# Kernel tuning notes

Hardware: AMD Instinct MI355X
Metric: run time of the kernel (lower is better)

The kernel has to match this reference:

```python
import jax, jax.numpy as jnp
import numpy as np

B, T, S = 32, 64, 64
V, E, H, Hs = 32000, 512, 512, 512
D2 = 2 * Hs  # src feature dim


def setup_inputs() -> dict:
    key = jax.random.key(0)
    ks = jax.random.split(key, 26)
    n = lambda k, shape, s=0.05: (jax.random.normal(k, shape, jnp.float32) * s)
    inp = {
        'src': jax.random.normal(ks[0], (B, S, D2), jnp.float32),
        'trg': jax.random.randint(ks[1], (B, T), 0, V),
        'mask': jnp.ones((B, T), jnp.float32),
        'emb': n(ks[2], (V, E)),
        # PyTorch LSTMCell params: weight_ih [4H, E+H], weight_hh [4H, H]
        'f_Wih': n(ks[3], (4 * H, E + H)), 'f_Whh': n(ks[4], (4 * H, H)),
        'f_bih': n(ks[5], (4 * H,)), 'f_bhh': n(ks[6], (4 * H,)),
        'b_Wih': n(ks[7], (4 * H, E + H)), 'b_Whh': n(ks[8], (4 * H, H)),
        'b_bih': n(ks[9], (4 * H,)), 'b_bhh': n(ks[10], (4 * H,)),
        # attention projections: hidden -> 2*src_hidden
        'fatt_W': n(ks[11], (D2, H)), 'fatt_b': n(ks[12], (D2,)),
        'batt_W': n(ks[13], (D2, H)), 'batt_b': n(ks[14], (D2,)),
        # att_hidden linears: (H + 2*Hs) -> H
        'fah_W': n(ks[15], (H, H + D2)), 'fah_b': n(ks[16], (H,)),
        'bah_W': n(ks[17], (H, H + D2)), 'bah_b': n(ks[18], (H,)),
        # output projection 2H -> V
        'fc_W': n(ks[19], (V, 2 * H)), 'fc_b': n(ks[20], (V,)),
        'feed_init': n(ks[21], (2 * H,), 1.0),
        'hid_init': n(ks[22], (4 * H,), 1.0),
    }
    return inp


def reference(src, trg, mask, emb, f_Wih, f_Whh, f_bih, f_bhh,
              b_Wih, b_Whh, b_bih, b_bhh, fatt_W, fatt_b, batt_W, batt_b,
              fah_W, fah_b, bah_W, bah_b, fc_W, fc_b, feed_init, hid_init):
    Bn = src.shape[0]
    Hn = feed_init.shape[0] // 2
    scale = 1.0 / np.sqrt(Hn)  # key.size(-1) == trg hidden before projection

    x = emb[trg]  # [B, T, E]  (dropout p=0 -> identity)

    hhat0 = jnp.broadcast_to(feed_init, (Bn, 2 * Hn))
    f_hhat0, b_hhat0 = jnp.split(hhat0, 2, axis=1)
    hid0 = jnp.broadcast_to(hid_init, (Bn, 4 * Hn))
    f_hid, b_hid = jnp.split(hid0, 2, axis=-1)
    f_h0, f_c0 = jnp.split(f_hid, 2, axis=-1)
    b_h0, b_c0 = jnp.split(b_hid, 2, axis=-1)

    def lstm(xin, h, c, Wih, Whh, bih, bhh):
        g = xin @ Wih.T + bih + h @ Whh.T + bhh
        i, f, gg, o = jnp.split(g, 4, axis=-1)
        c = jax.nn.sigmoid(f) * c + jax.nn.sigmoid(i) * jnp.tanh(gg)
        h = jax.nn.sigmoid(o) * jnp.tanh(c)
        return h, c

    def att(h, W, b):
        k = h @ W.T + b                              # [B, 2Hs]
        w = jnp.einsum('bd,bsd->bs', k, src) * scale  # [B, S]
        p = jax.nn.softmax(w, axis=-1)
        return jnp.einsum('bs,bsd->bd', p, src)       # [B, 2Hs]

    xs = jnp.swapaxes(x, 0, 1)      # [T, B, E]
    ms = jnp.swapaxes(mask, 0, 1)   # [T, B]

    def f_step(carry, x_t):
        h, c, hhat = carry
        h, c = lstm(jnp.concatenate([x_t, hhat], -1), h, c, f_Wih, f_Whh, f_bih, f_bhh)
        ct = att(h, fatt_W, fatt_b)
        # NOTE: original uses b_att_hidden in the forward loop (faithful)
        hhat = jnp.tanh(jnp.concatenate([h, ct], -1) @ bah_W.T + bah_b)
        return (h, c, hhat), hhat

    _, f_out = jax.lax.scan(f_step, (f_h0, f_c0, f_hhat0), xs)  # [T, B, H]

    def b_step(carry, inp):
        x_t, m_t = inp
        h, c, hhat = carry
        hn, cn = lstm(jnp.concatenate([x_t, hhat], -1), h, c, b_Wih, b_Whh, b_bih, b_bhh)
        h = m_t[:, None] * hn
        c = m_t[:, None] * cn
        ct = att(h, batt_W, batt_b)
        # NOTE: original uses f_att_hidden in the backward loop (faithful)
        hhat = jnp.tanh(jnp.concatenate([h, ct], -1) @ fah_W.T + fah_b)
        return (h, c, hhat), hhat

    _, b_out = jax.lax.scan(b_step, (b_h0, b_c0, b_hhat0), (xs[::-1], ms[::-1]))

    f_out = jnp.swapaxes(f_out, 0, 1)        # [B, T, H]
    b_cheat = jnp.swapaxes(b_out, 0, 1)      # reversed-time order, as stacked in torch
    # b_outputs[:, :-2] = b_outputs_cheat[:, 2:]; last two steps zero (faithful)
    b_shift = jnp.concatenate([b_cheat[:, 2:], jnp.zeros_like(b_cheat[:, :2])], axis=1)

    logits = jnp.concatenate([f_out, b_shift], -1) @ fc_W.T + fc_b  # [B, T, V]
    return logits
```

## Files before the change

kernel.cpp:

```cpp
#include <hip/hip_runtime.h>
#include <hip/hip_bf16.h>
#include <math.h>

typedef __hip_bfloat16 bf16;
typedef __attribute__((ext_vector_type(8))) short short8b;
typedef __attribute__((ext_vector_type(8))) __bf16 bf16x8;
typedef __attribute__((ext_vector_type(4))) float f32x4;
typedef __attribute__((ext_vector_type(2))) unsigned u32x2;

#define SCALE_F 0.04419417382415922f

template <typename V>
static __device__ inline auto mfma_try(V a, V b, f32x4 c, int)
    -> decltype(__builtin_amdgcn_mfma_f32_16x16x32_bf16(a, b, c, 0, 0, 0)) {
  return __builtin_amdgcn_mfma_f32_16x16x32_bf16(a, b, c, 0, 0, 0);
}
template <typename V>
static __device__ inline auto mfma_try(V a, V b, f32x4 c, long)
    -> decltype(__builtin_amdgcn_mfma_f32_16x16x32_bf16(
        __builtin_bit_cast(bf16x8, a), __builtin_bit_cast(bf16x8, b), c, 0, 0, 0)) {
  return __builtin_amdgcn_mfma_f32_16x16x32_bf16(
      __builtin_bit_cast(bf16x8, a), __builtin_bit_cast(bf16x8, b), c, 0, 0, 0);
}
static __device__ inline f32x4 MFMA(short8b a, short8b b, f32x4 c) {
  return mfma_try(a, b, c, 0);
}

static __device__ inline short8b ldb8(const bf16* p) {
  return *reinterpret_cast<const short8b*>(p);
}
static __device__ inline float b2f(bf16 v) { return __bfloat162float(v); }
static __device__ inline bf16 f2b(float v) { return __float2bfloat16(v); }
static __device__ inline float s2f(short s) {
  unsigned u = ((unsigned)(unsigned short)s) << 16;
  return __builtin_bit_cast(float, u);
}
static __device__ inline unsigned pack2(float lo, float hi) {
  const unsigned a = (unsigned)__builtin_bit_cast(unsigned short, f2b(lo));
  const unsigned b = (unsigned)__builtin_bit_cast(unsigned short, f2b(hi));
  return a | (b << 16);
}
static __device__ inline float sigm(float x) { return 1.f / (1.f + expf(-x)); }

static __device__ inline void st4_wt(bf16* p, float lo, float hi) {
  unsigned ud = pack2(lo, hi);
  asm volatile("global_store_dword %0, %1, off sc0 sc1" ::"v"(p), "v"(ud)
               : "memory");
}
static __device__ inline void st8_wt(bf16* p, f32x4 v) {
  u32x2 ud;
  ud[0] = pack2(v[0], v[1]);
  ud[1] = pack2(v[2], v[3]);
  asm volatile("global_store_dwordx2 %0, %1, off sc0 sc1" ::"v"(p), "v"(ud)
               : "memory");
}

static __device__ inline void st_flag(unsigned* p, unsigned v) {
  asm volatile("global_store_dword %0, %1, off sc0 sc1" ::"v"(p), "v"(v)
               : "memory");
}
static __device__ inline unsigned ld_flag(const unsigned* p) {
  unsigned v;
  asm volatile("global_load_dword %0, %1, off sc0 sc1\n\ts_waitcnt vmcnt(0)"
               : "=v"(v)
               : "v"(p)
               : "memory");
  return v;
}

static __device__ inline void ld8_dw(
    const unsigned* p0, const unsigned* p1, const unsigned* p2, const unsigned* p3,
    const unsigned* p4, const unsigned* p5, const unsigned* p6, const unsigned* p7,
    unsigned& o0, unsigned& o1, unsigned& o2, unsigned& o3,
    unsigned& o4, unsigned& o5, unsigned& o6, unsigned& o7) {
  asm volatile(
      "global_load_dword %0, %8, off sc0 sc1\n\t"
      "global_load_dword %1, %9, off sc0 sc1\n\t"
      "global_load_dword %2, %10, off sc0 sc1\n\t"
      "global_load_dword %3, %11, off sc0 sc1\n\t"
      "global_load_dword %4, %12, off sc0 sc1\n\t"
      "global_load_dword %5, %13, off sc0 sc1\n\t"
      "global_load_dword %6, %14, off sc0 sc1\n\t"
      "global_load_dword %7, %15, off sc0 sc1"
      : "=&v"(o0), "=&v"(o1), "=&v"(o2), "=&v"(o3),
        "=&v"(o4), "=&v"(o5), "=&v"(o6), "=&v"(o7)
      : "v"(p0), "v"(p1), "v"(p2), "v"(p3), "v"(p4), "v"(p5), "v"(p6), "v"(p7)
      : "memory");
}

static __device__ inline void gbar(unsigned* flags, unsigned ep, int blk, int tid) {
  asm volatile("s_waitcnt vmcnt(0)" ::: "memory");
  __syncthreads();
  if (tid < 64) {
    unsigned* row = flags + (size_t)ep * 64;
    if (tid == 0) st_flag(row + blk, 1u);
    while (true) {
      const unsigned v = ld_flag(row + tid);
      if (__ballot(v != 0) == ~0ull) break;
      __builtin_amdgcn_s_sleep(1);
    }
  }
  __syncthreads();
}

template <typename OutT, bool HAS_BIAS>
__global__ __launch_bounds__(256) void gemm_k(
    const bf16* __restrict__ A, const bf16* __restrict__ Bw,
    OutT* __restrict__ C, const float* __restrict__ bias,
    int M, int N, int K) {
  const int lane = threadIdx.x & 63;
  const int wid = threadIdx.x >> 6;
  const int m0 = blockIdx.y * 128 + (wid >> 1) * 64;
  const int n0 = blockIdx.x * 128 + (wid & 1) * 64;
  const int lr = lane & 15;
  const int lk = (lane >> 4) * 8;
  f32x4 acc[4][4];
#pragma unroll
  for (int i = 0; i < 4; ++i)
#pragma unroll
    for (int j = 0; j < 4; ++j) acc[i][j] = (f32x4){0.f, 0.f, 0.f, 0.f};
  const bf16* Ap = A + (size_t)(m0 + lr) * K + lk;
  const bf16* Bp = Bw + (size_t)(n0 + lr) * K + lk;
  for (int k0 = 0; k0 < K; k0 += 32) {
    short8b av[4], bv[4];
#pragma unroll
    for (int i = 0; i < 4; ++i) av[i] = ldb8(Ap + (size_t)i * 16 * K + k0);
#pragma unroll
    for (int i = 0; i < 4; ++i) bv[i] = ldb8(Bp + (size_t)i * 16 * K + k0);
#pragma unroll
    for (int mi = 0; mi < 4; ++mi)
#pragma unroll
      for (int ni = 0; ni < 4; ++ni)
        acc[mi][ni] = MFMA(av[mi], bv[ni], acc[mi][ni]);
  }
  const int rb = (lane >> 4) * 4;
#pragma unroll
  for (int mi = 0; mi < 4; ++mi) {
#pragma unroll
    for (int r = 0; r < 4; ++r) {
      const int row = m0 + mi * 16 + rb + r;
#pragma unroll
      for (int ni = 0; ni < 4; ++ni) {
        const int col = n0 + ni * 16 + lr;
        float v = acc[mi][ni][r];
        if (HAS_BIAS) v += bias[col];
        if constexpr (sizeof(OutT) == 2) {
          C[(size_t)row * N + col] = f2b(v);
        } else {
          C[(size_t)row * N + col] = v;
        }
      }
    }
  }
}

__global__ __launch_bounds__(256) void gemm_out(
    const bf16* __restrict__ A, const bf16* __restrict__ Bw,
    float* __restrict__ C, const float* __restrict__ bias) {
  constexpr int K = 1024, N = 32000;
  __shared__ bf16 As[128 * 32];
  __shared__ bf16 Bs[128 * 32];
  const int wgid = blockIdx.x;
  const int mt = wgid & 15, nt = wgid >> 4;
  const int tid = threadIdx.x, lane = tid & 63, wv = tid >> 6;
  const int m0 = mt * 128, n0 = nt * 128;
  const int lr16 = lane & 15, kb = lane >> 4, koff = kb * 8;
  const int r0 = tid >> 2, q0 = tid & 3;
  const int r1 = (tid + 256) >> 2;
  const bf16* Ap0 = A + (size_t)(m0 + r0) * K + q0 * 8;
  const bf16* Ap1 = A + (size_t)(m0 + r1) * K + q0 * 8;
  const bf16* Bp0 = Bw + (size_t)(n0 + r0) * K + q0 * 8;
  const bf16* Bp1 = Bw + (size_t)(n0 + r1) * K + q0 * 8;
  const int wm = (wv >> 1) * 64, wn = (wv & 1) * 64;
  f32x4 acc[4][4];
#pragma unroll
  for (int i = 0; i < 4; ++i)
#pragma unroll
    for (int j = 0; j < 4; ++j) acc[i][j] = (f32x4){0.f, 0.f, 0.f, 0.f};
  short8b a0 = ldb8(Ap0), a1 = ldb8(Ap1), b0 = ldb8(Bp0), b1 = ldb8(Bp1);
  for (int k0 = 0; k0 < K; k0 += 32) {
    __syncthreads();
    *reinterpret_cast<short8b*>(&As[tid * 8]) = a0;
    *reinterpret_cast<short8b*>(&As[(tid + 256) * 8]) = a1;
    *reinterpret_cast<short8b*>(&Bs[tid * 8]) = b0;
    *reinterpret_cast<short8b*>(&Bs[(tid + 256) * 8]) = b1;
    __syncthreads();
    if (k0 + 32 < K) {
      a0 = ldb8(Ap0 + k0 + 32);
      a1 = ldb8(Ap1 + k0 + 32);
      b0 = ldb8(Bp0 + k0 + 32);
      b1 = ldb8(Bp1 + k0 + 32);
    }
    short8b af[4], bfr[4];
#pragma unroll
    for (int i = 0; i < 4; ++i) {
      af[i] = *reinterpret_cast<const short8b*>(&As[(wm + i * 16 + lr16) * 32 + koff]);
      bfr[i] = *reinterpret_cast<const short8b*>(&Bs[(wn + i * 16 + lr16) * 32 + koff]);
    }
#pragma unroll
    for (int mi = 0; mi < 4; ++mi)
#pragma unroll
      for (int ni = 0; ni < 4; ++ni)
        acc[mi][ni] = MFMA(af[mi], bfr[ni], acc[mi][ni]);
  }
#pragma unroll
  for (int mi = 0; mi < 4; ++mi) {
#pragma unroll
    for (int r = 0; r < 4; ++r) {
      const int row = m0 + wm + mi * 16 + kb * 4 + r;
#pragma unroll
      for (int ni = 0; ni < 4; ++ni) {
        const int col = n0 + wn + ni * 16 + lr16;
        C[(size_t)row * N + col] = acc[mi][ni][r] + bias[col];
      }
    }
  }
}

__global__ void k_xg(const float* __restrict__ emb, const int* __restrict__ trg,
                     bf16* __restrict__ xg) {
  const int i = blockIdx.x * 256 + threadIdx.x;
  const int r = i >> 9, e = i & 511;
  const int t = r >> 5, b = r & 31;
  const int tok = trg[b * 64 + t];
  xg[i] = f2b(emb[(size_t)tok * 512 + e]);
}

__global__ void k_srcb(const float* __restrict__ s, bf16* __restrict__ d) {
  const int i = blockIdx.x * 256 + threadIdx.x;
  d[i] = f2b(s[i]);
}

__global__ void k_fcw(const float* __restrict__ s, bf16* __restrict__ d) {
  const size_t stride = (size_t)gridDim.x * blockDim.x;
  for (size_t i = blockIdx.x * (size_t)blockDim.x + threadIdx.x;
       i < (size_t)32000 * 1024; i += stride)
    d[i] = f2b(s[i]);
}

__global__ void k_bmt(const bf16* __restrict__ in, bf16* __restrict__ out) {
  const int i = blockIdx.x * 256 + threadIdx.x;
  const int b = i >> 15, rem = i & 32767, o = rem >> 6, s = rem & 63;
  out[i] = in[(size_t)(b * 64 + s) * 512 + o];
}

__global__ void k_wpack(const float* __restrict__ fWih, const float* __restrict__ fWhh,
                        const float* __restrict__ bWih, const float* __restrict__ bWhh,
                        const float* __restrict__ fattW, const float* __restrict__ battW,
                        const float* __restrict__ bahW, const float* __restrict__ fahW,
                        bf16* Wxf, bf16* Wxb, bf16* Wrecf, bf16* Wrecb,
                        bf16* attWtf, bf16* attWtb, bf16* ahW2f, bf16* ahW2b,
                        bf16* Wh1f, bf16* Wh1b) {
  const int stride = gridDim.x * blockDim.x;
  const int i0 = blockIdx.x * blockDim.x + threadIdx.x;
  for (int i = i0; i < 2048 * 512; i += stride) {
    const int gc = i >> 9, k = i & 511;
    Wxf[i] = f2b(fWih[(size_t)gc * 1024 + k]);
    Wxb[i] = f2b(bWih[(size_t)gc * 1024 + k]);
  }
  for (int i = i0; i < 2048 * 1024; i += stride) {
    const int gc = i >> 10, k = i & 1023;
    float vf, vb;
    if (k < 512) { vf = fWih[(size_t)gc * 1024 + 512 + k]; vb = bWih[(size_t)gc * 1024 + 512 + k]; }
    else         { vf = fWhh[(size_t)gc * 512 + k - 512]; vb = bWhh[(size_t)gc * 512 + k - 512]; }
    Wrecf[i] = f2b(vf); Wrecb[i] = f2b(vb);
  }
  for (int i = i0; i < 512 * 1024; i += stride) {
    const int j = i >> 10, d = i & 1023;
    attWtf[i] = f2b(fattW[(size_t)d * 512 + j]);
    attWtb[i] = f2b(battW[(size_t)d * 512 + j]);
  }
  for (int i = i0; i < 512 * 1024; i += stride) {
    const int o = i >> 10, d = i & 1023;
    ahW2f[i] = f2b(bahW[(size_t)o * 1536 + 512 + d]);
    ahW2b[i] = f2b(fahW[(size_t)o * 1536 + 512 + d]);
  }
  for (int i = i0; i < 512 * 512; i += stride) {
    const int o = i >> 9, k = i & 511;
    Wh1f[i] = f2b(bahW[(size_t)o * 1536 + k]);
    Wh1b[i] = f2b(fahW[(size_t)o * 1536 + k]);
  }
}

__global__ void k_c0(const float* __restrict__ src, const float* __restrict__ fb,
                     const float* __restrict__ bb, float* __restrict__ c0f,
                     float* __restrict__ c0b) {
  const int r = blockIdx.x;
  const int tid = threadIdx.x;
  float pf = 0.f, pb = 0.f;
  for (int d = tid; d < 1024; d += 256) {
    const float s = src[(size_t)r * 1024 + d];
    pf += s * fb[d];
    pb += s * bb[d];
  }
#pragma unroll
  for (int d = 1; d < 64; d <<= 1) { pf += __shfl_xor(pf, d); pb += __shfl_xor(pb, d); }
  __shared__ float rf[4], rb2[4];
  if ((tid & 63) == 0) { rf[tid >> 6] = pf; rb2[tid >> 6] = pb; }
  __syncthreads();
  if (tid == 0) {
    c0f[r] = (rf[0] + rf[1] + rf[2] + rf[3]) * SCALE_F;
    c0b[r] = (rb2[0] + rb2[1] + rb2[2] + rb2[3]) * SCALE_F;
  }
}

__global__ void k_init(const float* __restrict__ feed, const float* __restrict__ hid,
                       bf16* hh0, bf16* hh1, bf16* hb0, bf16* hb1,
                       float* cst0, float* cst1) {
  const int i = blockIdx.x * 256 + threadIdx.x;
  const int b = i >> 9, k = i & 511;
  hh0[i] = f2b(feed[k]);
  hh1[i] = f2b(feed[512 + k]);
  hb0[i] = f2b(hid[k]);
  hb1[i] = f2b(hid[1024 + k]);
  cst0[k * 32 + b] = hid[512 + k];
  cst1[k * 32 + b] = hid[1536 + k];
}

struct ScanP {
  const bf16* Wrec[2]; const bf16* Xp[2]; const bf16* Af[2]; const bf16* Bmt[2];
  const bf16* Wh1[2]; const float* bih[2]; const float* bhh[2];
  const float* c0[2]; const float* ahb[2]; const float* mask;
  bf16* hh[2]; bf16* hb[2]; bf16* Up[2]; float* cst[2]; bf16* hcat; unsigned* flags;
};

__global__ __launch_bounds__(256) void scan_k(ScanP P) {
  const int blk = blockIdx.x;
  const int dir = blk >> 5;
  const int g = blk & 31;
  const int tid = threadIdx.x;
  const int lane = tid & 63;
  const int wv = tid >> 6;

  const bf16* __restrict__ Wrec = P.Wrec[dir];
  const bf16* __restrict__ Xp = P.Xp[dir];
  const bf16* __restrict__ Af = P.Af[dir];
  const bf16* __restrict__ Bmt = P.Bmt[dir];
  const bf16* __restrict__ Wh1 = P.Wh1[dir];
  const float* __restrict__ bihp = P.bih[dir];
  const float* __restrict__ bhhp = P.bhh[dir];
  const float* __restrict__ c0v = P.c0[dir];
  const float* __restrict__ ahbp = P.ahb[dir];
  bf16* __restrict__ hhB = P.hh[dir];
  bf16* __restrict__ hbB = P.hb[dir];
  bf16* __restrict__ Up = P.Up[dir];
  float* __restrict__ cst = P.cst[dir];

  __shared__ float gl[4][16][33];
  __shared__ bf16 hs[32][16];
  __shared__ float h_lds[512];
  __shared__ float w_part[4][64];
  __shared__ float p_lds[64];

  unsigned ep = 0;
  const int lr16 = lane & 15;
  const int kb = lane >> 4;
  const int koff = kb * 8;

  short8b pA0[16], pA1[16];
  {
    const bf16* A0 = hbB + (size_t)lr16 * 512;
    const bf16* A1 = hbB + (size_t)(lr16 + 16) * 512;
#pragma unroll
    for (int ks = 0; ks < 16; ++ks) {
      pA0[ks] = ldb8(A0 + ks * 32 + koff);
      pA1[ks] = ldb8(A1 + ks * 32 + koff);
    }
  }

  for (int t = 0; t < 64; ++t) {
    const bf16* hhR = hhB + (size_t)t * 32 * 512;
    bf16* hhW = hhB + (size_t)(t + 1) * 32 * 512;
    bf16* hbW = hbB + (size_t)(t + 1) * 32 * 512;

    {
      const int gate = wv;
      const int gc = gate * 512 + g * 16 + lr16;
      const bf16* Brow = Wrec + (size_t)gc * 1024;
      const bf16* A0h = hhR + (size_t)lr16 * 512;
      const bf16* A1h = hhR + (size_t)(lr16 + 16) * 512;
      f32x4 ac0 = (f32x4){0.f, 0.f, 0.f, 0.f};
      f32x4 ac1 = (f32x4){0.f, 0.f, 0.f, 0.f};
#pragma unroll
      for (int ks = 0; ks < 16; ++ks) {
        const int k = ks * 32 + koff;
        const short8b bv = ldb8(Brow + 512 + k);
        ac0 = MFMA(pA0[ks], bv, ac0);
        ac1 = MFMA(pA1[ks], bv, ac1);
      }
#pragma unroll
      for (int c = 0; c < 2; ++c) {
        short8b sa[8], sb[8];
#pragma unroll
        for (int i = 0; i < 8; ++i) {
          const int k = (c * 8 + i) * 32 + koff;
          sa[i] = ldb8(A0h + k);
          sb[i] = ldb8(A1h + k);
        }
#pragma unroll
        for (int i = 0; i < 8; ++i) {
          const int k = (c * 8 + i) * 32 + koff;
          const short8b bv = ldb8(Brow + k);
          ac0 = MFMA(sa[i], bv, ac0);
          ac1 = MFMA(sb[i], bv, ac1);
        }
      }
      const int tcol = dir ? (63 - t) : t;
      const float bsum = bihp[gc] + bhhp[gc];
      const bf16* xpc = Xp + (size_t)gc * 2048 + tcol * 32;
#pragma unroll
      for (int r = 0; r < 4; ++r) {
        const int brow = kb * 4 + r;
        gl[gate][lr16][brow] = ac0[r] + b2f(xpc[brow]) + bsum;
        gl[gate][lr16][brow + 16] = ac1[r] + b2f(xpc[brow + 16]) + bsum;
      }
    }
    __syncthreads();
    {
      const int b = tid & 31;
      const int jp = (tid >> 5) * 2;
      float hn2[2];
#pragma unroll
      for (int u = 0; u < 2; ++u) {
        const int jl = jp + u;
        const int j = g * 16 + jl;
        const float gi = gl[0][jl][b];
        const float gf = gl[1][jl][b];
        const float gg = gl[2][jl][b];
        const float go = gl[3][jl][b];
        float cn = sigm(gf) * cst[j * 32 + b] + sigm(gi) * tanhf(gg);
        float hn = sigm(go) * tanhf(cn);
        if (dir) {
          const float m = P.mask[b * 64 + (63 - t)];
          hn *= m; cn *= m;
        }
        cst[j * 32 + b] = cn;
        hn2[u] = hn;
      }
      st4_wt(hbW + (size_t)b * 512 + g * 16 + jp, hn2[0], hn2[1]);
      *reinterpret_cast<unsigned*>(&hs[b][jp]) = pack2(hn2[0], hn2[1]);
    }
    __syncthreads();
    {
      short8b hx0 = {0, 0, 0, 0, 0, 0, 0, 0};
      short8b hx1 = {0, 0, 0, 0, 0, 0, 0, 0};
      if (kb < 2) {
        hx0 = *reinterpret_cast<const short8b*>(&hs[lr16][kb * 8]);
        hx1 = *reinterpret_cast<const short8b*>(&hs[lr16 + 16][kb * 8]);
      }
      const f32x4 zac = (f32x4){0.f, 0.f, 0.f, 0.f};
      bf16* Ug = Up + (size_t)g * 32 * 512;
#pragma unroll
      for (int oi = 0; oi < 8; ++oi) {
        const int og = wv + oi * 4;
        short8b yv = {0, 0, 0, 0, 0, 0, 0, 0};
        if (kb < 2)
          yv = ldb8(Wh1 + (size_t)(og * 16 + lr16) * 512 + g * 16 + kb * 8);
        const f32x4 u0 = MFMA(yv, hx0, zac);
        const f32x4 u1 = MFMA(yv, hx1, zac);
        const int oo = og * 16 + kb * 4;
        st8_wt(Ug + (size_t)lr16 * 512 + oo, u0);
        st8_wt(Ug + (size_t)(lr16 + 16) * 512 + oo, u1);
      }
    }
    gbar(P.flags, ep++, blk, tid);

    if (tid < 64) {
      const short8b v = ldb8(hbW + (size_t)g * 512 + tid * 8);
#pragma unroll
      for (int e = 0; e < 8; ++e) h_lds[tid * 8 + e] = s2f(v[e]);
    }
    __syncthreads();
    {
      const int q = wv;
      const bf16* arow = Af + (size_t)(g * 64 + lane) * 512 + q * 128;
      float part = 0.f;
#pragma unroll 8
      for (int k8 = 0; k8 < 128; k8 += 8) {
        const short8b v = ldb8(arow + k8);
#pragma unroll
        for (int e = 0; e < 8; ++e) part += h_lds[q * 128 + k8 + e] * s2f(v[e]);
      }
      w_part[q][lane] = part;
    }
    __syncthreads();
    if (wv == 3) {
      const float v = (w_part[0][lane] + w_part[1][lane] + w_part[2][lane] +
                       w_part[3][lane]) * SCALE_F + c0v[g * 64 + lane];
      float mx = v;
#pragma unroll
      for (int d = 1; d < 64; d <<= 1) mx = fmaxf(mx, __shfl_xor(mx, d));
      const float e = expf(v - mx);
      float sm = e;
#pragma unroll
      for (int d = 1; d < 64; d <<= 1) sm += __shfl_xor(sm, d);
      p_lds[lane] = e / sm;
    }
    __syncthreads();
    {
      const int o2 = tid * 2;
      const unsigned* ub = reinterpret_cast<const unsigned*>(Up) + g * 256 + tid;
      unsigned d[32];
#pragma unroll
      for (int q4 = 0; q4 < 4; ++q4) {
        ld8_dw(ub + (q4 * 8 + 0) * 8192, ub + (q4 * 8 + 1) * 8192,
               ub + (q4 * 8 + 2) * 8192, ub + (q4 * 8 + 3) * 8192,
               ub + (q4 * 8 + 4) * 8192, ub + (q4 * 8 + 5) * 8192,
               ub + (q4 * 8 + 6) * 8192, ub + (q4 * 8 + 7) * 8192,
               d[q4 * 8 + 0], d[q4 * 8 + 1], d[q4 * 8 + 2], d[q4 * 8 + 3],
               d[q4 * 8 + 4], d[q4 * 8 + 5], d[q4 * 8 + 6], d[q4 * 8 + 7]);
      }
      float s0 = ahbp[o2], s1 = ahbp[o2 + 1];
      {
        const bf16* bm0 = Bmt + ((size_t)g * 512 + o2) * 64;
        short8b v0[8], v1[8];
#pragma unroll
        for (int i = 0; i < 8; ++i) {
          v0[i] = ldb8(bm0 + i * 8);
          v1[i] = ldb8(bm0 + 64 + i * 8);
        }
#pragma unroll
        for (int i = 0; i < 8; ++i)
#pragma unroll
          for (int e = 0; e < 8; ++e) {
            const float p = p_lds[i * 8 + e];
            s0 += p * s2f(v0[i][e]);
            s1 += p * s2f(v1[i][e]);
          }
      }
      asm volatile("s_waitcnt vmcnt(0)" ::: "memory");
      float u0 = 0.f, u1 = 0.f;
#pragma unroll
      for (int i = 0; i < 32; ++i) {
        u0 += s2f((short)(d[i] & 0xffffu));
        u1 += s2f((short)(d[i] >> 16));
      }
      const float h0 = tanhf(s0 + u0);
      const float h1 = tanhf(s1 + u1);
      st4_wt(hhW + (size_t)g * 512 + o2, h0, h1);
      const unsigned hp = pack2(h0, h1);
      if (dir == 0) {
        *reinterpret_cast<unsigned*>(P.hcat + (size_t)(g * 64 + t) * 1024 + o2) = hp;
      } else if (t >= 2) {
        *reinterpret_cast<unsigned*>(P.hcat + (size_t)(g * 64 + t - 2) * 1024 + 512 + o2) = hp;
      }
      if (t < 63) {
        const bf16* A0 = hbW + (size_t)lr16 * 512;
        const bf16* A1 = hbW + (size_t)(lr16 + 16) * 512;
#pragma unroll
        for (int ks = 0; ks < 16; ++ks) {
          pA0[ks] = ldb8(A0 + ks * 32 + koff);
          pA1[ks] = ldb8(A1 + ks * 32 + koff);
        }
      }
    }
    gbar(P.flags, ep++, blk, tid);
  }
}

extern "C" void kernel_launch(void* const* d_in, const int* in_sizes, int n_in,
                              void* d_out, int out_size, void* d_ws, size_t ws_size,
                              hipStream_t stream) {
  (void)in_sizes; (void)n_in; (void)out_size; (void)ws_size;
  const float* src  = (const float*)d_in[0];
  const int*   trg  = (const int*)d_in[1];
  const float* mask = (const float*)d_in[2];
  const float* emb  = (const float*)d_in[3];
  const float* fWih = (const float*)d_in[4];
  const float* fWhh = (const float*)d_in[5];
  const float* fbih = (const float*)d_in[6];
  const float* fbhh = (const float*)d_in[7];
  const float* bWih = (const float*)d_in[8];
  const float* bWhh = (const float*)d_in[9];
  const float* bbih = (const float*)d_in[10];
  const float* bbhh = (const float*)d_in[11];
  const float* fattW = (const float*)d_in[12];
  const float* fattb = (const float*)d_in[13];
  const float* battW = (const float*)d_in[14];
  const float* battb = (const float*)d_in[15];
  const float* fahW = (const float*)d_in[16];
  const float* fahb = (const float*)d_in[17];
  const float* bahW = (const float*)d_in[18];
  const float* bahb = (const float*)d_in[19];
  const float* fcW  = (const float*)d_in[20];
  const float* fcb  = (const float*)d_in[21];
  const float* feed = (const float*)d_in[22];
  const float* hid  = (const float*)d_in[23];

  char* wsp = (char*)d_ws;
  size_t off = 0;
  auto alloc = [&](size_t bytes) -> void* {
    void* p = wsp + off;
    off += (bytes + 255) & ~(size_t)255;
    return p;
  };
  unsigned* flags = (unsigned*)alloc((size_t)192 * 64 * 4);
  bf16* hcat = (bf16*)alloc((size_t)2048 * 1024 * 2);
  const size_t zero_bytes = off;
  bf16* xg    = (bf16*)alloc((size_t)2048 * 512 * 2);
  bf16* srcb  = (bf16*)alloc((size_t)2048 * 1024 * 2);
  bf16* fcWb  = (bf16*)alloc((size_t)32000 * 1024 * 2);
  bf16* Wxf   = (bf16*)alloc((size_t)2048 * 512 * 2);
  bf16* Wxb   = (bf16*)alloc((size_t)2048 * 512 * 2);
  bf16* Wrecf = (bf16*)alloc((size_t)2048 * 1024 * 2);
  bf16* Wrecb = (bf16*)alloc((size_t)2048 * 1024 * 2);
  bf16* attWtf = (bf16*)alloc((size_t)512 * 1024 * 2);
  bf16* attWtb = (bf16*)alloc((size_t)512 * 1024 * 2);
  bf16* ahW2f = (bf16*)alloc((size_t)512 * 1024 * 2);
  bf16* ahW2b = (bf16*)alloc((size_t)512 * 1024 * 2);
  bf16* Wh1f  = (bf16*)alloc((size_t)512 * 512 * 2);
  bf16* Wh1b  = (bf16*)alloc((size_t)512 * 512 * 2);
  bf16* Xpf   = (bf16*)alloc((size_t)2048 * 2048 * 2);
  bf16* Xpb   = (bf16*)alloc((size_t)2048 * 2048 * 2);
  bf16* Aff   = (bf16*)alloc((size_t)2048 * 512 * 2);
  bf16* Afb   = (bf16*)alloc((size_t)2048 * 512 * 2);
  bf16* Bmf   = (bf16*)alloc((size_t)2048 * 512 * 2);
  bf16* Bmb   = (bf16*)alloc((size_t)2048 * 512 * 2);
  bf16* Bmtf  = (bf16*)alloc((size_t)2048 * 512 * 2);
  bf16* Bmtb  = (bf16*)alloc((size_t)2048 * 512 * 2);
  bf16* Upf   = (bf16*)alloc((size_t)32 * 32 * 512 * 2);
  bf16* Upb   = (bf16*)alloc((size_t)32 * 32 * 512 * 2);
  float* c0f  = (float*)alloc(2048 * 4);
  float* c0b  = (float*)alloc(2048 * 4);
  bf16* hh0   = (bf16*)alloc((size_t)65 * 32 * 512 * 2);
  bf16* hh1   = (bf16*)alloc((size_t)65 * 32 * 512 * 2);
  bf16* hb0   = (bf16*)alloc((size_t)65 * 32 * 512 * 2);
  bf16* hb1   = (bf16*)alloc((size_t)65 * 32 * 512 * 2);
  float* cst0 = (float*)alloc((size_t)512 * 32 * 4);
  float* cst1 = (float*)alloc((size_t)512 * 32 * 4);

  hipMemsetAsync(d_ws, 0, zero_bytes, stream);

  k_xg<<<4096, 256, 0, stream>>>(emb, trg, xg);
  k_srcb<<<8192, 256, 0, stream>>>(src, srcb);
  k_fcw<<<8192, 256, 0, stream>>>(fcW, fcWb);
  k_wpack<<<2048, 256, 0, stream>>>(fWih, fWhh, bWih, bWhh, fattW, battW, bahW, fahW,
                                    Wxf, Wxb, Wrecf, Wrecb, attWtf, attWtb, ahW2f, ahW2b,
                                    Wh1f, Wh1b);
  k_c0<<<2048, 256, 0, stream>>>(src, fattb, battb, c0f, c0b);
  k_init<<<64, 256, 0, stream>>>(feed, hid, hh0, hh1, hb0, hb1, cst0, cst1);

  gemm_k<bf16, false><<<dim3(16, 16), 256, 0, stream>>>(Wxf, xg, Xpf, nullptr, 2048, 2048, 512);
  gemm_k<bf16, false><<<dim3(16, 16), 256, 0, stream>>>(Wxb, xg, Xpb, nullptr, 2048, 2048, 512);
  gemm_k<bf16, false><<<dim3(4, 16), 256, 0, stream>>>(srcb, attWtf, Aff, nullptr, 2048, 512, 1024);
  gemm_k<bf16, false><<<dim3(4, 16), 256, 0, stream>>>(srcb, attWtb, Afb, nullptr, 2048, 512, 1024);
  gemm_k<bf16, false><<<dim3(4, 16), 256, 0, stream>>>(srcb, ahW2f, Bmf, nullptr, 2048, 512, 1024);
  gemm_k<bf16, false><<<dim3(4, 16), 256, 0, stream>>>(srcb, ahW2b, Bmb, nullptr, 2048, 512, 1024);
  k_bmt<<<4096, 256, 0, stream>>>(Bmf, Bmtf);
  k_bmt<<<4096, 256, 0, stream>>>(Bmb, Bmtb);

  ScanP sp;
  sp.Wrec[0] = Wrecf; sp.Wrec[1] = Wrecb;
  sp.Xp[0] = Xpf;     sp.Xp[1] = Xpb;
  sp.Af[0] = Aff;     sp.Af[1] = Afb;
  sp.Bmt[0] = Bmtf;   sp.Bmt[1] = Bmtb;
  sp.Wh1[0] = Wh1f;   sp.Wh1[1] = Wh1b;
  sp.bih[0] = fbih;   sp.bih[1] = bbih;
  sp.bhh[0] = fbhh;   sp.bhh[1] = bbhh;
  sp.c0[0] = c0f;     sp.c0[1] = c0b;
  sp.ahb[0] = bahb;   sp.ahb[1] = fahb;
  sp.mask = mask;
  sp.hh[0] = hh0;     sp.hh[1] = hh1;
  sp.hb[0] = hb0;     sp.hb[1] = hb1;
  sp.Up[0] = Upf;     sp.Up[1] = Upb;
  sp.cst[0] = cst0;   sp.cst[1] = cst1;
  sp.hcat = hcat;     sp.flags = flags;
  scan_k<<<64, 256, 0, stream>>>(sp);

  gemm_out<<<4000, 256, 0, stream>>>(hcat, fcWb, (float*)d_out, fcb);
}
```

Before: 2.378 ms.

## Double-buffer output GEMM with direct global-to-LDS loads; fuse Bm transpose into GEMM

The vocabulary projection GEMM now uses two LDS buffers filled by global_load_lds, so the next K-slice streams into shared memory while MFMAs run on the current one. This removes the register staging and one barrier per iteration. Separately, the Bm GEMMs write their output directly in the transposed 64-row layout, which removes the two k_bmt transpose kernels and the intermediate buffers. The cost is doubled LDS use in the output GEMM and scattered stores in the transposed GEMM epilogue.

```diff
diff --git a/kernel.cpp b/kernel.cpp
--- a/kernel.cpp
+++ b/kernel.cpp
@@ -41,6 +41,12 @@
   return a | (b << 16);
 }
 static __device__ inline float sigm(float x) { return 1.f / (1.f + expf(-x)); }
+
+static __device__ inline void gl_lds16(const bf16* g, bf16* l) {
+  __builtin_amdgcn_global_load_lds(
+      (const __attribute__((address_space(1))) void*)g,
+      (__attribute__((address_space(3))) void*)l, 16, 0, 0);
+}
 
 static __device__ inline void st4_wt(bf16* p, float lo, float hi) {
   unsigned ud = pack2(lo, hi);
@@ -103,7 +109,7 @@
   __syncthreads();
 }
 
-template <typename OutT, bool HAS_BIAS>
+template <typename OutT, bool HAS_BIAS, bool TRANS64 = false>
 __global__ __launch_bounds__(256) void gemm_k(
     const bf16* __restrict__ A, const bf16* __restrict__ Bw,
     OutT* __restrict__ C, const float* __restrict__ bias,
@@ -144,7 +150,9 @@
         const int col = n0 + ni * 16 + lr;
         float v = acc[mi][ni][r];
         if (HAS_BIAS) v += bias[col];
-        if constexpr (sizeof(OutT) == 2) {
+        if constexpr (TRANS64) {
+          C[((size_t)(row >> 6) * N + col) * 64 + (row & 63)] = f2b(v);
+        } else if constexpr (sizeof(OutT) == 2) {
           C[(size_t)row * N + col] = f2b(v);
         } else {
           C[(size_t)row * N + col] = v;
@@ -158,50 +166,54 @@
     const bf16* __restrict__ A, const bf16* __restrict__ Bw,
     float* __restrict__ C, const float* __restrict__ bias) {
   constexpr int K = 1024, N = 32000;
-  __shared__ bf16 As[128 * 32];
-  __shared__ bf16 Bs[128 * 32];
+  __shared__ bf16 As[2][128 * 32];
+  __shared__ bf16 Bs[2][128 * 32];
   const int wgid = blockIdx.x;
   const int mt = wgid & 15, nt = wgid >> 4;
   const int tid = threadIdx.x, lane = tid & 63, wv = tid >> 6;
   const int m0 = mt * 128, n0 = nt * 128;
   const int lr16 = lane & 15, kb = lane >> 4, koff = kb * 8;
-  const int r0 = tid >> 2, q0 = tid & 3;
-  const int r1 = (tid + 256) >> 2;
-  const bf16* Ap0 = A + (size_t)(m0 + r0) * K + q0 * 8;
-  const bf16* Ap1 = A + (size_t)(m0 + r1) * K + q0 * 8;
-  const bf16* Bp0 = Bw + (size_t)(n0 + r0) * K + q0 * 8;
-  const bf16* Bp1 = Bw + (size_t)(n0 + r1) * K + q0 * 8;
   const int wm = (wv >> 1) * 64, wn = (wv & 1) * 64;
+  const int c0 = wv * 64 + lane;
+  const int c1 = c0 + 256;
+  const bf16* gA0 = A + (size_t)(m0 + (c0 >> 2)) * K + (c0 & 3) * 8;
+  const bf16* gA1 = A + (size_t)(m0 + (c1 >> 2)) * K + (c1 & 3) * 8;
+  const bf16* gB0 = Bw + (size_t)(n0 + (c0 >> 2)) * K + (c0 & 3) * 8;
+  const bf16* gB1 = Bw + (size_t)(n0 + (c1 >> 2)) * K + (c1 & 3) * 8;
+  const int ldsOffA = wv * 512;
   f32x4 acc[4][4];
 #pragma unroll
   for (int i = 0; i < 4; ++i)
 #pragma unroll
     for (int j = 0; j < 4; ++j) acc[i][j] = (f32x4){0.f, 0.f, 0.f, 0.f};
-  short8b a0 = ldb8(Ap0), a1 = ldb8(Ap1), b0 = ldb8(Bp0), b1 = ldb8(Bp1);
+  gl_lds16(gA0, &As[0][ldsOffA]);
+  gl_lds16(gA1, &As[0][ldsOffA + 2048]);
+  gl_lds16(gB0, &Bs[0][ldsOffA]);
+  gl_lds16(gB1, &Bs[0][ldsOffA + 2048]);
+  asm volatile("s_waitcnt vmcnt(0)" ::: "memory");
+  __syncthreads();
+  int buf = 0;
   for (int k0 = 0; k0 < K; k0 += 32) {
-    __syncthreads();
-    *reinterpret_cast<short8b*>(&As[tid * 8]) = a0;
-    *reinterpret_cast<short8b*>(&As[(tid + 256) * 8]) = a1;
-    *reinterpret_cast<short8b*>(&Bs[tid * 8]) = b0;
-    *reinterpret_cast<short8b*>(&Bs[(tid + 256) * 8]) = b1;
-    __syncthreads();
     if (k0 + 32 < K) {
-      a0 = ldb8(Ap0 + k0 + 32);
-      a1 = ldb8(Ap1 + k0 + 32);
-      b0 = ldb8(Bp0 + k0 + 32);
-      b1 = ldb8(Bp1 + k0 + 32);
+      gl_lds16(gA0 + k0 + 32, &As[buf ^ 1][ldsOffA]);
+      gl_lds16(gA1 + k0 + 32, &As[buf ^ 1][ldsOffA + 2048]);
+      gl_lds16(gB0 + k0 + 32, &Bs[buf ^ 1][ldsOffA]);
+      gl_lds16(gB1 + k0 + 32, &Bs[buf ^ 1][ldsOffA + 2048]);
     }
     short8b af[4], bfr[4];
 #pragma unroll
     for (int i = 0; i < 4; ++i) {
-      af[i] = *reinterpret_cast<const short8b*>(&As[(wm + i * 16 + lr16) * 32 + koff]);
-      bfr[i] = *reinterpret_cast<const short8b*>(&Bs[(wn + i * 16 + lr16) * 32 + koff]);
+      af[i] = *reinterpret_cast<const short8b*>(&As[buf][(wm + i * 16 + lr16) * 32 + koff]);
+      bfr[i] = *reinterpret_cast<const short8b*>(&Bs[buf][(wn + i * 16 + lr16) * 32 + koff]);
     }
 #pragma unroll
     for (int mi = 0; mi < 4; ++mi)
 #pragma unroll
       for (int ni = 0; ni < 4; ++ni)
         acc[mi][ni] = MFMA(af[mi], bfr[ni], acc[mi][ni]);
+    asm volatile("s_waitcnt vmcnt(0)" ::: "memory");
+    __syncthreads();
+    buf ^= 1;
   }
 #pragma unroll
   for (int mi = 0; mi < 4; ++mi) {
@@ -236,12 +248,6 @@
   for (size_t i = blockIdx.x * (size_t)blockDim.x + threadIdx.x;
        i < (size_t)32000 * 1024; i += stride)
     d[i] = f2b(s[i]);
-}
-
-__global__ void k_bmt(const bf16* __restrict__ in, bf16* __restrict__ out) {
-  const int i = blockIdx.x * 256 + threadIdx.x;
-  const int b = i >> 15, rem = i & 32767, o = rem >> 6, s = rem & 63;
-  out[i] = in[(size_t)(b * 64 + s) * 512 + o];
 }
 
 __global__ void k_wpack(const float* __restrict__ fWih, const float* __restrict__ fWhh,
@@ -614,8 +620,6 @@
   bf16* Xpb   = (bf16*)alloc((size_t)2048 * 2048 * 2);
   bf16* Aff   = (bf16*)alloc((size_t)2048 * 512 * 2);
   bf16* Afb   = (bf16*)alloc((size_t)2048 * 512 * 2);
-  bf16* Bmf   = (bf16*)alloc((size_t)2048 * 512 * 2);
-  bf16* Bmb   = (bf16*)alloc((size_t)2048 * 512 * 2);
   bf16* Bmtf  = (bf16*)alloc((size_t)2048 * 512 * 2);
   bf16* Bmtb  = (bf16*)alloc((size_t)2048 * 512 * 2);
   bf16* Upf   = (bf16*)alloc((size_t)32 * 32 * 512 * 2);
@@ -644,10 +648,8 @@
   gemm_k<bf16, false><<<dim3(16, 16), 256, 0, stream>>>(Wxb, xg, Xpb, nullptr, 2048, 2048, 512);
   gemm_k<bf16, false><<<dim3(4, 16), 256, 0, stream>>>(srcb, attWtf, Aff, nullptr, 2048, 512, 1024);
   gemm_k<bf16, false><<<dim3(4, 16), 256, 0, stream>>>(srcb, attWtb, Afb, nullptr, 2048, 512, 1024);
-  gemm_k<bf16, false><<<dim3(4, 16), 256, 0, stream>>>(srcb, ahW2f, Bmf, nullptr, 2048, 512, 1024);
-  gemm_k<bf16, false><<<dim3(4, 16), 256, 0, stream>>>(srcb, ahW2b, Bmb, nullptr, 2048, 512, 1024);
-  k_bmt<<<4096, 256, 0, stream>>>(Bmf, Bmtf);
-  k_bmt<<<4096, 256, 0, stream>>>(Bmb, Bmtb);
+  gemm_k<bf16, false, true><<<dim3(4, 16), 256, 0, stream>>>(srcb, ahW2f, Bmtf, nullptr, 2048, 512, 1024);
+  gemm_k<bf16, false, true><<<dim3(4, 16), 256, 0, stream>>>(srcb, ahW2b, Bmtb, nullptr, 2048, 512, 1024);
 
   ScanP sp;
   sp.Wrec[0] = Wrecf; sp.Wrec[1] = Wrecb;
```

Result: no change. 2.391 ms (+0.6%).
